# Optimization experiments

Measured on AMD Instinct MI355X. Metric: run time of the kernel, lower is better.

The kernel has to match this reference:

```python
import jax, jax.numpy as jnp
import numpy as np

B, S, D, H = 4, 1024, 512, 8
DH = D // H  # d_head = 64
SQRT_DIM = float(np.sqrt(D))


def _rel_shift(pos_score):
    # pos_score: [B, H, S1, S2] -> Transformer-XL relative shift
    b, h, s1, s2 = pos_score.shape
    padded = jnp.pad(pos_score, ((0, 0), (0, 0), (0, 0), (1, 0)))  # [B,H,S1,S2+1]
    padded = padded.reshape(b, h, s2 + 1, s1)
    return padded[:, :, 1:].reshape(b, h, s1, s2)


def setup_inputs() -> dict:
    key = jax.random.key(0)
    ks = jax.random.split(key, 16)
    p = lambda k, shape: (jax.random.normal(k, shape, dtype=jnp.float32) * 0.02)
    inp = {
        "inputs_1": jax.random.normal(ks[0], (B, S, D), dtype=jnp.float32),
        "inputs_2": jax.random.normal(ks[1], (B, S, D), dtype=jnp.float32),
        "pos_embedding": jax.random.normal(ks[2], (B, S, D), dtype=jnp.float32),
        "mask": jnp.zeros((B, 1, S), dtype=bool),
        "Wq": p(ks[3], (D, H * DH)), "bq": jnp.zeros((H * DH,), jnp.float32),
        "Wk": p(ks[4], (D, H * DH)), "bk": jnp.zeros((H * DH,), jnp.float32),
        "Wv": p(ks[5], (D, H * DH)), "bv": jnp.zeros((H * DH,), jnp.float32),
        "Wp": p(ks[6], (D, D)),  # pos_proj, no bias
        "u_bias": p(ks[7], (H, DH)),
        "v_bias": p(ks[8], (H, DH)),
        "Wo1": p(ks[9], (D, D)), "bo1": jnp.zeros((D,), jnp.float32),
        "Wo2": p(ks[10], (D, D)), "bo2": jnp.zeros((D,), jnp.float32),
    }
    return inp


def _stream(x, pos, mask, Wq, bq, Wk, bk, Wv, bv, u_bias, v_bias, Wo, bo):
    b = x.shape[0]
    q = (x @ Wq + bq).reshape(b, -1, H, DH)          # [B,S,H,dh]
    k = (x @ Wk + bk).reshape(b, -1, H, DH)          # [B,S,H,dh]
    v = (x @ Wv + bv).reshape(b, -1, H, DH)          # [B,S,H,dh]
    content = jnp.einsum("bshd,bthd->bhst", q + u_bias, k)
    pos_score = jnp.einsum("bshd,bthd->bhst", q + v_bias, pos)
    pos_score = _rel_shift(pos_score)
    score = (content + pos_score) / SQRT_DIM          # [B,H,S,S]
    if mask is not None:
        score = jnp.where(mask[:, None], -1e9, score)  # mask: [B,1,S]->[B,1,1,S]
    attn = jax.nn.softmax(score, axis=-1)
    ctx = jnp.einsum("bhst,bthd->bshd", attn, v).reshape(b, -1, D)
    ctx = ctx @ Wo + bo
    return ctx, attn


def reference(inputs_1, inputs_2, pos_embedding, mask, Wq, bq, Wk, bk, Wv, bv,
              Wp, u_bias, v_bias, Wo1, bo1, Wo2, bo2):
    b = inputs_1.shape[0]
    pos = (pos_embedding @ Wp).reshape(b, -1, H, DH)  # [B,S,H,dh]
    # NOTE: original torch code uses value_proj_1 for BOTH streams (value_proj_2 unused)
    ctx1, attn1 = _stream(inputs_1, pos, mask, Wq, bq, Wk, bk, Wv, bv,
                          u_bias, v_bias, Wo1, bo1)
    ctx2, attn2 = _stream(inputs_2, pos, mask, Wq, bq, Wk, bk, Wv, bv,
                          u_bias, v_bias, Wo2, bo2)
    return (ctx1, attn1, ctx2, attn2)
```

## Files before the change

kernel.cpp:

```cpp
#include <hip/hip_runtime.h>
#include <hip/hip_bf16.h>
#include <stdint.h>

typedef __attribute__((ext_vector_type(4))) float f32x4;
typedef __attribute__((ext_vector_type(8))) short bf16x8;

#define OFF_X1B   0UL
#define OFF_X2B   4194304UL
#define OFF_PEB   8388608UL
#define OFF_WQT   12582912UL
#define OFF_WKT   13107200UL
#define OFF_WVT   13631488UL
#define OFF_WPT   14155776UL
#define OFF_WO1T  14680064UL
#define OFF_WO2T  15204352UL
#define OFF_QU1   15728640UL
#define OFF_QV1   19922944UL
#define OFF_K1    24117248UL
#define OFF_V1    28311552UL
#define OFF_QU2   32505856UL
#define OFF_QV2   36700160UL
#define OFF_K2    40894464UL
#define OFF_V2    45088768UL
#define OFF_POSP  49283072UL
#define OFF_VT1   53477376UL
#define OFF_VT2   57671680UL
#define OFF_CP1   61865984UL
#define OFF_CP2   66060288UL

#define CTX1_OFF  0UL
#define ATTN1_OFF 2097152UL
#define CTX2_OFF  35651584UL
#define ATTN2_OFF 37748736UL

struct PP {
  const float* x1; const float* x2; const float* pe; const unsigned char* mask;
  const float* Wq; const float* bq; const float* Wk; const float* bk;
  const float* Wv; const float* bv; const float* Wp;
  const float* ub; const float* vb;
  const float* Wo1; const float* bo1; const float* Wo2; const float* bo2;
  float* out; char* ws;
};

__device__ __forceinline__ short f2bf(float f){
  union { float f; unsigned u; } v; v.f = f;
  unsigned r = v.u + 0x7FFFu + ((v.u >> 16) & 1u);
  return (short)(r >> 16);
}
__device__ __forceinline__ float bf2f(short s){
  union { unsigned u; float f; } v; v.u = ((unsigned)(unsigned short)s) << 16;
  return v.f;
}

__global__ __launch_bounds__(256) void k_cvt(PP p){
  int z = blockIdx.y;
  const float* s = (z==0) ? p.x1 : (z==1) ? p.x2 : p.pe;
  short* d = (short*)(p.ws + (z==0 ? OFF_X1B : z==1 ? OFF_X2B : OFF_PEB));
  size_t i = ((size_t)(blockIdx.x*256 + threadIdx.x))*8;
  float4 a = *(const float4*)(s+i);
  float4 b = *(const float4*)(s+i+4);
  bf16x8 o;
  o[0]=f2bf(a.x); o[1]=f2bf(a.y); o[2]=f2bf(a.z); o[3]=f2bf(a.w);
  o[4]=f2bf(b.x); o[5]=f2bf(b.y); o[6]=f2bf(b.z); o[7]=f2bf(b.w);
  *(bf16x8*)(d+i) = o;
}

__global__ __launch_bounds__(256) void k_cvtw(PP p){
  int z = blockIdx.y;
  const float* src = (z==0)?p.Wq:(z==1)?p.Wk:(z==2)?p.Wv:(z==3)?p.Wp:(z==4)?p.Wo1:p.Wo2;
  short* dst = (short*)(p.ws + ((z==0)?OFF_WQT:(z==1)?OFF_WKT:(z==2)?OFF_WVT:(z==3)?OFF_WPT:(z==4)?OFF_WO1T:OFF_WO2T));
  int tile = blockIdx.x;
  int k0 = (tile & 7)*64, n0 = (tile >> 3)*64;
  __shared__ short tl[64][68];
  int t = threadIdx.x;
  int i = t>>2, jc = (t&3)*16;
  const float* s = src + (size_t)(k0+i)*512 + n0 + jc;
  #pragma unroll
  for (int q=0;q<16;q+=4){
    float4 v = *(const float4*)(s+q);
    tl[i][jc+q+0]=f2bf(v.x); tl[i][jc+q+1]=f2bf(v.y);
    tl[i][jc+q+2]=f2bf(v.z); tl[i][jc+q+3]=f2bf(v.w);
  }
  __syncthreads();
  int n = t>>2, kp2 = (t&3)*16;
  bf16x8 o0, o1;
  #pragma unroll
  for (int q=0;q<8;q++){ o0[q] = tl[kp2+q][n]; o1[q] = tl[kp2+8+q][n]; }
  short* dp = dst + (size_t)(n0+n)*512 + k0 + kp2;
  *(bf16x8*)dp = o0;
  *(bf16x8*)(dp+8) = o1;
}

__global__ __launch_bounds__(256) void k_gemm(PP p, int job_base){
  const int job = job_base + blockIdx.z;
  char* ws = p.ws;
  const short *A, *BT; const float* bias = nullptr;
  short* o0 = nullptr; const float* eb0 = nullptr;
  short* o1 = nullptr; const float* eb1 = nullptr;
  float* of = nullptr;
  switch(job){
    case 0: A=(const short*)(ws+OFF_X1B); BT=(const short*)(ws+OFF_WQT); bias=p.bq;
            o0=(short*)(ws+OFF_QU1); eb0=p.ub; o1=(short*)(ws+OFF_QV1); eb1=p.vb; break;
    case 1: A=(const short*)(ws+OFF_X1B); BT=(const short*)(ws+OFF_WKT); bias=p.bk; o0=(short*)(ws+OFF_K1); break;
    case 2: A=(const short*)(ws+OFF_X1B); BT=(const short*)(ws+OFF_WVT); bias=p.bv; o0=(short*)(ws+OFF_V1); break;
    case 3: A=(const short*)(ws+OFF_X2B); BT=(const short*)(ws+OFF_WQT); bias=p.bq;
            o0=(short*)(ws+OFF_QU2); eb0=p.ub; o1=(short*)(ws+OFF_QV2); eb1=p.vb; break;
    case 4: A=(const short*)(ws+OFF_X2B); BT=(const short*)(ws+OFF_WKT); bias=p.bk; o0=(short*)(ws+OFF_K2); break;
    case 5: A=(const short*)(ws+OFF_X2B); BT=(const short*)(ws+OFF_WVT); bias=p.bv; o0=(short*)(ws+OFF_V2); break;
    case 6: A=(const short*)(ws+OFF_PEB); BT=(const short*)(ws+OFF_WPT); o0=(short*)(ws+OFF_POSP); break;
    case 7: A=(const short*)(ws+OFF_CP1); BT=(const short*)(ws+OFF_WO1T); bias=p.bo1; of=p.out + CTX1_OFF; break;
    default: A=(const short*)(ws+OFF_CP2); BT=(const short*)(ws+OFF_WO2T); bias=p.bo2; of=p.out + CTX2_OFF; break;
  }
  __shared__ short As[128][72];
  __shared__ short Bs[128][72];
  const int t = threadIdx.x, w = t>>6, l = t&63, g = l>>4, r = l&15;
  const int m0 = blockIdx.x*128, n0 = blockIdx.y*128;
  const int wm = (w>>1)*64, wn = (w&1)*64;
  f32x4 acc[4][4];
  #pragma unroll
  for (int i=0;i<4;i++)
    #pragma unroll
    for(int j=0;j<4;j++) acc[i][j] = (f32x4){0.f,0.f,0.f,0.f};

  for (int k0=0; k0<512; k0+=64){
    __syncthreads();
    #pragma unroll
    for (int i=0;i<4;i++){
      int c = t + 256*i;
      int row = c>>3, kc = (c&7)*8;
      *(bf16x8*)&As[row][kc] = *(const bf16x8*)(A + (size_t)(m0+row)*512 + k0 + kc);
      *(bf16x8*)&Bs[row][kc] = *(const bf16x8*)(BT + (size_t)(n0+row)*512 + k0 + kc);
    }
    __syncthreads();
    #pragma unroll
    for (int kk=0; kk<64; kk+=32){
      bf16x8 a[4], bb[4];
      #pragma unroll
      for (int i=0;i<4;i++) a[i] = *(const bf16x8*)&As[wm+16*i+r][kk+8*g];
      #pragma unroll
      for (int j=0;j<4;j++) bb[j] = *(const bf16x8*)&Bs[wn+16*j+r][kk+8*g];
      #pragma unroll
      for (int i=0;i<4;i++)
        #pragma unroll
        for (int j=0;j<4;j++)
          acc[i][j] = __builtin_amdgcn_mfma_f32_16x16x32_bf16(a[i], bb[j], acc[i][j], 0,0,0);
    }
  }
  #pragma unroll
  for (int i=0;i<4;i++){
    #pragma unroll
    for (int j=0;j<4;j++){
      int col = n0 + wn + 16*j + r;
      float bv = bias ? bias[col] : 0.f;
      float e0 = eb0 ? eb0[col] : 0.f;
      float e1 = eb1 ? eb1[col] : 0.f;
      #pragma unroll
      for (int rr=0; rr<4; rr++){
        size_t row = (size_t)(m0 + wm + 16*i + 4*g + rr);
        float val = acc[i][j][rr] + bv;
        if (of) of[row*512 + col] = val;
        else {
          o0[row*512 + col] = f2bf(val + e0);
          if (o1) o1[row*512 + col] = f2bf(val + e1);
        }
      }
    }
  }
}

__global__ __launch_bounds__(256) void k_vtrans(PP p){
  int stile = blockIdx.x, bh = blockIdx.y, st = blockIdx.z;
  const short* v = (const short*)(p.ws + (st? OFF_V2:OFF_V1));
  short* vT = (short*)(p.ws + (st? OFF_VT2:OFF_VT1));
  int b = bh>>3, h = bh&7;
  __shared__ short tl[64][68];
  int t = threadIdx.x;
  int i = t>>2, jc = (t&3)*16;
  const short* src = v + ((size_t)(b*1024 + stile*64 + i))*512 + h*64 + jc;
  *(bf16x8*)&tl[i][jc]   = *(const bf16x8*)src;
  *(bf16x8*)&tl[i][jc+8] = *(const bf16x8*)(src+8);
  __syncthreads();
  int d = t>>2, sp = (t&3)*16;
  bf16x8 o0, o1;
  #pragma unroll
  for (int q=0;q<8;q++){ o0[q]=tl[sp+q][d]; o1[q]=tl[sp+8+q][d]; }
  short* dp = vT + ((size_t)(bh*64 + d))*1024 + stile*64 + sp;
  *(bf16x8*)dp = o0;
  *(bf16x8*)(dp+8) = o1;
}

__global__ __launch_bounds__(256) void k_attn(PP p){
  const int t = threadIdx.x, w = t>>6, l = t&63, g = l>>4, r = l&15;
  const int qt = blockIdx.x, bh = blockIdx.y, st = blockIdx.z;
  const int b = bh>>3, h = bh&7;
  const int r0 = qt*16;
  char* ws = p.ws;
  const short* qu = (const short*)(ws + (st? OFF_QU2:OFF_QU1));
  const short* qv = (const short*)(ws + (st? OFF_QV2:OFF_QV1));
  const short* kp = (const short*)(ws + (st? OFF_K2:OFF_K1));
  const short* vT = (const short*)(ws + (st? OFF_VT2:OFF_VT1));
  short* cp = (short*)(ws + (st? OFF_CP2:OFF_CP1));
  float* attn_out = p.out + (st? ATTN2_OFF : ATTN1_OFF);
  const short* posp = (const short*)(ws + OFF_POSP);

  union ScBuf { short ps[17][1024]; float sc[16][1024]; };
  __shared__ ScBuf u;

  bf16x8 aqu[2], aqv[2], aqv2[2];
  {
    size_t base = ((size_t)(b*1024 + r0 + r))*512 + h*64 + 8*g;
    int row2 = r0 + 16 + r; if (row2 > 1023) row2 = 1023;
    size_t base2 = ((size_t)(b*1024 + row2))*512 + h*64 + 8*g;
    #pragma unroll
    for (int ks=0; ks<2; ks++){
      aqu[ks]  = *(const bf16x8*)(qu + base  + ks*32);
      aqv[ks]  = *(const bf16x8*)(qv + base  + ks*32);
      aqv2[ks] = *(const bf16x8*)(qv + base2 + ks*32);
    }
  }

  {
    size_t pbase = ((size_t)(b*1024))*512 + h*64 + 8*g;
    #pragma unroll 4
    for (int tt=0; tt<16; tt++){
      int n = 256*w + 16*tt;
      f32x4 a0 = {0.f,0.f,0.f,0.f}, a1 = {0.f,0.f,0.f,0.f};
      #pragma unroll
      for (int ks=0; ks<2; ks++){
        bf16x8 bf = *(const bf16x8*)(posp + pbase + (size_t)(n + r)*512 + ks*32);
        a0 = __builtin_amdgcn_mfma_f32_16x16x32_bf16(aqv[ks],  bf, a0, 0,0,0);
        a1 = __builtin_amdgcn_mfma_f32_16x16x32_bf16(aqv2[ks], bf, a1, 0,0,0);
      }
      #pragma unroll
      for (int rr=0; rr<4; rr++) u.ps[4*g+rr][n+r] = f2bf(a0[rr]);
      if (g==0) u.ps[16][n+r] = f2bf(a1[0]);
    }
  }
  __syncthreads();

  f32x4 sca[16];
  {
    size_t kbase = ((size_t)(b*1024))*512 + h*64 + 8*g;
    const unsigned char* mk = p.mask + b*1024;
    #pragma unroll 4
    for (int tt=0; tt<16; tt++){
      int n = 256*w + 16*tt;
      f32x4 a0 = {0.f,0.f,0.f,0.f};
      #pragma unroll
      for (int ks=0; ks<2; ks++){
        bf16x8 bf = *(const bf16x8*)(kp + kbase + (size_t)(n + r)*512 + ks*32);
        a0 = __builtin_amdgcn_mfma_f32_16x16x32_bf16(aqu[ks], bf, a0, 0,0,0);
      }
      int s2 = n + r;
      bool msk = (mk[s2] != 0);
      #pragma unroll
      for (int rr=0; rr<4; rr++){
        int lr = 4*g + rr;
        int s1 = r0 + lr;
        float pv;
        if (s2 <= s1)        pv = bf2f(u.ps[lr][s2 + 1023 - s1]);
        else if (s2 == s1+1) pv = 0.f;
        else                 pv = bf2f(u.ps[lr+1][s2 - s1 - 2]);
        float sv = (a0[rr] + pv) * 0.04419417382415922f;
        if (msk) sv = -1e9f;
        sca[tt][rr] = sv;
      }
    }
  }
  __syncthreads();

  #pragma unroll
  for (int tt=0; tt<16; tt++){
    int s2 = 256*w + 16*tt + r;
    #pragma unroll
    for (int rr=0; rr<4; rr++){
      int row = 4*g + rr;
      u.sc[row][s2 ^ ((row&7)<<3)] = sca[tt][rr];
    }
  }
  __syncthreads();

  #pragma unroll
  for (int rr=0; rr<4; rr++){
    int row = 4*w + rr;
    int sw = (row&7)<<3;
    float vals[16];
    float mx = -1e30f;
    #pragma unroll
    for (int j=0;j<16;j++){
      vals[j] = u.sc[row][(l + 64*j) ^ sw];
      mx = fmaxf(mx, vals[j]);
    }
    #pragma unroll
    for (int off=32; off>0; off>>=1) mx = fmaxf(mx, __shfl_xor(mx, off));
    float s = 0.f;
    #pragma unroll
    for (int j=0;j<16;j++){ vals[j] = __expf(vals[j]-mx); s += vals[j]; }
    #pragma unroll
    for (int off=32; off>0; off>>=1) s += __shfl_xor(s, off);
    float inv = 1.f / s;
    size_t gb = (((size_t)(b*8 + h))*1024 + (size_t)(r0 + row))*1024;
    #pragma unroll
    for (int j=0;j<16;j++){
      float a = vals[j]*inv;
      u.sc[row][(l + 64*j) ^ sw] = a;
      attn_out[gb + l + 64*j] = a;
    }
  }
  __syncthreads();

  {
    f32x4 acc = {0.f,0.f,0.f,0.f};
    const short* vrow = vT + ((size_t)(bh*64 + 16*w + r))*1024;
    int sw = (r&7)<<3;
    for (int k0=0; k0<1024; k0+=32){
      int kb = (k0 + 8*g) ^ sw;
      const float* ap = &u.sc[r][kb];
      f32x4 f0 = *(const f32x4*)ap;
      f32x4 f1 = *(const f32x4*)(ap+4);
      bf16x8 af;
      af[0]=f2bf(f0[0]); af[1]=f2bf(f0[1]); af[2]=f2bf(f0[2]); af[3]=f2bf(f0[3]);
      af[4]=f2bf(f1[0]); af[5]=f2bf(f1[1]); af[6]=f2bf(f1[2]); af[7]=f2bf(f1[3]);
      bf16x8 bf = *(const bf16x8*)(vrow + k0 + 8*g);
      acc = __builtin_amdgcn_mfma_f32_16x16x32_bf16(af, bf, acc, 0,0,0);
    }
    size_t obase = ((size_t)(b*1024 + r0))*512 + (size_t)(h*64 + 16*w + r);
    #pragma unroll
    for (int rr=0; rr<4; rr++)
      cp[obase + (size_t)(4*g+rr)*512] = f2bf(acc[rr]);
  }
}

extern "C" void kernel_launch(void* const* d_in, const int* in_sizes, int n_in,
                              void* d_out, int out_size, void* d_ws, size_t ws_size,
                              hipStream_t stream){
  PP p;
  p.x1  = (const float*)d_in[0];
  p.x2  = (const float*)d_in[1];
  p.pe  = (const float*)d_in[2];
  p.mask= (const unsigned char*)d_in[3];
  p.Wq  = (const float*)d_in[4];  p.bq = (const float*)d_in[5];
  p.Wk  = (const float*)d_in[6];  p.bk = (const float*)d_in[7];
  p.Wv  = (const float*)d_in[8];  p.bv = (const float*)d_in[9];
  p.Wp  = (const float*)d_in[10];
  p.ub  = (const float*)d_in[11]; p.vb = (const float*)d_in[12];
  p.Wo1 = (const float*)d_in[13]; p.bo1= (const float*)d_in[14];
  p.Wo2 = (const float*)d_in[15]; p.bo2= (const float*)d_in[16];
  p.out = (float*)d_out;
  p.ws  = (char*)d_ws;

  hipLaunchKernelGGL(k_cvt,    dim3(1024,3), dim3(256), 0, stream, p);
  hipLaunchKernelGGL(k_cvtw,   dim3(64,6),   dim3(256), 0, stream, p);
  hipLaunchKernelGGL(k_gemm,   dim3(32,4,7), dim3(256), 0, stream, p, 0);
  hipLaunchKernelGGL(k_vtrans, dim3(16,32,2),dim3(256), 0, stream, p);
  hipLaunchKernelGGL(k_attn,   dim3(64,32,2),dim3(256), 0, stream, p);
  hipLaunchKernelGGL(k_gemm,   dim3(32,4,2), dim3(256), 0, stream, p, 7);
}
```

Before: 657.2 us.

## Fuse content and position MFMAs, keep softmax in registers, store probabilities as bf16 in LDS

Computes the content score (q+u)·k in the same loop as the positional score, so k and pos tiles are loaded together. Softmax now runs directly on the MFMA accumulator registers, using shuffle plus a small LDS cross-wave reduction instead of staging a 64KB float score buffer through shared memory. The normalized probabilities are written to global with nontemporal stores and stored as bf16 into the reused swizzled pos buffer, so the PV MFMA loads bf16 operands directly. This shrinks LDS from 64KB to about 34KB, which should allow more resident blocks, and removes one barrier-and-copy stage. The cost is higher register pressure from full unrolling.

```diff
diff --git a/kernel.cpp b/kernel.cpp
--- a/kernel.cpp
+++ b/kernel.cpp
@@ -203,8 +203,10 @@
   float* attn_out = p.out + (st? ATTN2_OFF : ATTN1_OFF);
   const short* posp = (const short*)(ws + OFF_POSP);
 
-  union ScBuf { short ps[17][1024]; float sc[16][1024]; };
-  __shared__ ScBuf u;
+  __shared__ short ps[17*1024];
+  __shared__ float red[2][4][16];
+
+  #define PSI(row,col) ((row)*1024 + ((col) ^ (((row)&7)<<3)))
 
   bf16x8 aqu[2], aqv[2], aqv2[2];
   {
@@ -219,92 +221,114 @@
     }
   }
 
+  f32x4 sca[16];
   {
     size_t pbase = ((size_t)(b*1024))*512 + h*64 + 8*g;
-    #pragma unroll 4
+    #pragma unroll
     for (int tt=0; tt<16; tt++){
       int n = 256*w + 16*tt;
-      f32x4 a0 = {0.f,0.f,0.f,0.f}, a1 = {0.f,0.f,0.f,0.f};
+      f32x4 c0 = {0.f,0.f,0.f,0.f}, p0 = {0.f,0.f,0.f,0.f}, p1 = {0.f,0.f,0.f,0.f};
       #pragma unroll
       for (int ks=0; ks<2; ks++){
-        bf16x8 bf = *(const bf16x8*)(posp + pbase + (size_t)(n + r)*512 + ks*32);
-        a0 = __builtin_amdgcn_mfma_f32_16x16x32_bf16(aqv[ks],  bf, a0, 0,0,0);
-        a1 = __builtin_amdgcn_mfma_f32_16x16x32_bf16(aqv2[ks], bf, a1, 0,0,0);
+        size_t off = pbase + (size_t)(n + r)*512 + ks*32;
+        bf16x8 pf = *(const bf16x8*)(posp + off);
+        bf16x8 kf = *(const bf16x8*)(kp + off);
+        p0 = __builtin_amdgcn_mfma_f32_16x16x32_bf16(aqv[ks],  pf, p0, 0,0,0);
+        p1 = __builtin_amdgcn_mfma_f32_16x16x32_bf16(aqv2[ks], pf, p1, 0,0,0);
+        c0 = __builtin_amdgcn_mfma_f32_16x16x32_bf16(aqu[ks],  kf, c0, 0,0,0);
       }
-      #pragma unroll
-      for (int rr=0; rr<4; rr++) u.ps[4*g+rr][n+r] = f2bf(a0[rr]);
-      if (g==0) u.ps[16][n+r] = f2bf(a1[0]);
-    }
-  }
-  __syncthreads();
-
-  f32x4 sca[16];
-  {
-    size_t kbase = ((size_t)(b*1024))*512 + h*64 + 8*g;
+      sca[tt] = c0;
+      #pragma unroll
+      for (int rr=0; rr<4; rr++) ps[PSI(4*g+rr, n+r)] = f2bf(p0[rr]);
+      if (g==0) ps[PSI(16, n+r)] = f2bf(p1[0]);
+    }
+  }
+  __syncthreads();
+
+  {
     const unsigned char* mk = p.mask + b*1024;
-    #pragma unroll 4
+    #pragma unroll
     for (int tt=0; tt<16; tt++){
       int n = 256*w + 16*tt;
-      f32x4 a0 = {0.f,0.f,0.f,0.f};
-      #pragma unroll
-      for (int ks=0; ks<2; ks++){
-        bf16x8 bf = *(const bf16x8*)(kp + kbase + (size_t)(n + r)*512 + ks*32);
-        a0 = __builtin_amdgcn_mfma_f32_16x16x32_bf16(aqu[ks], bf, a0, 0,0,0);
-      }
       int s2 = n + r;
       bool msk = (mk[s2] != 0);
       #pragma unroll
       for (int rr=0; rr<4; rr++){
-        int lr = 4*g + rr;
-        int s1 = r0 + lr;
+        int lr = 4*g + rr, s1 = r0 + lr;
         float pv;
-        if (s2 <= s1)        pv = bf2f(u.ps[lr][s2 + 1023 - s1]);
+        if (s2 <= s1)        pv = bf2f(ps[PSI(lr, s2 + 1023 - s1)]);
         else if (s2 == s1+1) pv = 0.f;
-        else                 pv = bf2f(u.ps[lr+1][s2 - s1 - 2]);
-        float sv = (a0[rr] + pv) * 0.04419417382415922f;
+        else                 pv = bf2f(ps[PSI(lr+1, s2 - s1 - 2)]);
+        float sv = (sca[tt][rr] + pv) * 0.04419417382415922f;
         if (msk) sv = -1e9f;
         sca[tt][rr] = sv;
       }
     }
   }
-  __syncthreads();
-
+
+  float mx[4];
+  #pragma unroll
+  for (int rr=0; rr<4; rr++){
+    float m_ = -1e30f;
+    #pragma unroll
+    for (int tt=0; tt<16; tt++) m_ = fmaxf(m_, sca[tt][rr]);
+    mx[rr] = m_;
+  }
+  #pragma unroll
+  for (int off=1; off<16; off<<=1){
+    #pragma unroll
+    for (int rr=0; rr<4; rr++) mx[rr] = fmaxf(mx[rr], __shfl_xor(mx[rr], off));
+  }
+  if (r==0){
+    #pragma unroll
+    for (int rr=0; rr<4; rr++) red[0][w][4*g+rr] = mx[rr];
+  }
+  __syncthreads();
+  #pragma unroll
+  for (int rr=0; rr<4; rr++){
+    int lr = 4*g + rr;
+    mx[rr] = fmaxf(fmaxf(red[0][0][lr], red[0][1][lr]),
+                   fmaxf(red[0][2][lr], red[0][3][lr]));
+  }
+  float sm[4] = {0.f,0.f,0.f,0.f};
   #pragma unroll
   for (int tt=0; tt<16; tt++){
-    int s2 = 256*w + 16*tt + r;
     #pragma unroll
     for (int rr=0; rr<4; rr++){
-      int row = 4*g + rr;
-      u.sc[row][s2 ^ ((row&7)<<3)] = sca[tt][rr];
-    }
-  }
-  __syncthreads();
-
+      float e = __expf(sca[tt][rr] - mx[rr]);
+      sca[tt][rr] = e;
+      sm[rr] += e;
+    }
+  }
+  #pragma unroll
+  for (int off=1; off<16; off<<=1){
+    #pragma unroll
+    for (int rr=0; rr<4; rr++) sm[rr] += __shfl_xor(sm[rr], off);
+  }
+  if (r==0){
+    #pragma unroll
+    for (int rr=0; rr<4; rr++) red[1][w][4*g+rr] = sm[rr];
+  }
+  __syncthreads();
+  float inv[4];
   #pragma unroll
   for (int rr=0; rr<4; rr++){
-    int row = 4*w + rr;
-    int sw = (row&7)<<3;
-    float vals[16];
-    float mx = -1e30f;
-    #pragma unroll
-    for (int j=0;j<16;j++){
-      vals[j] = u.sc[row][(l + 64*j) ^ sw];
-      mx = fmaxf(mx, vals[j]);
-    }
-    #pragma unroll
-    for (int off=32; off>0; off>>=1) mx = fmaxf(mx, __shfl_xor(mx, off));
-    float s = 0.f;
-    #pragma unroll
-    for (int j=0;j<16;j++){ vals[j] = __expf(vals[j]-mx); s += vals[j]; }
-    #pragma unroll
-    for (int off=32; off>0; off>>=1) s += __shfl_xor(s, off);
-    float inv = 1.f / s;
-    size_t gb = (((size_t)(b*8 + h))*1024 + (size_t)(r0 + row))*1024;
-    #pragma unroll
-    for (int j=0;j<16;j++){
-      float a = vals[j]*inv;
-      u.sc[row][(l + 64*j) ^ sw] = a;
-      attn_out[gb + l + 64*j] = a;
+    int lr = 4*g + rr;
+    inv[rr] = 1.f / (red[1][0][lr] + red[1][1][lr] + red[1][2][lr] + red[1][3][lr]);
+  }
+
+  {
+    size_t gbase = ((size_t)(b*8 + h))*1048576 + (size_t)r0*1024;
+    #pragma unroll
+    for (int tt=0; tt<16; tt++){
+      int n = 256*w + 16*tt;
+      #pragma unroll
+      for (int rr=0; rr<4; rr++){
+        int lr = 4*g + rr;
+        float a = sca[tt][rr] * inv[rr];
+        __builtin_nontemporal_store(a, &attn_out[gbase + (size_t)lr*1024 + n + r]);
+        ps[PSI(lr, n + r)] = f2bf(a);
+      }
     }
   }
   __syncthreads();
@@ -312,15 +336,9 @@
   {
     f32x4 acc = {0.f,0.f,0.f,0.f};
     const short* vrow = vT + ((size_t)(bh*64 + 16*w + r))*1024;
-    int sw = (r&7)<<3;
+    #pragma unroll 8
     for (int k0=0; k0<1024; k0+=32){
-      int kb = (k0 + 8*g) ^ sw;
-      const float* ap = &u.sc[r][kb];
-      f32x4 f0 = *(const f32x4*)ap;
-      f32x4 f1 = *(const f32x4*)(ap+4);
-      bf16x8 af;
-      af[0]=f2bf(f0[0]); af[1]=f2bf(f0[1]); af[2]=f2bf(f0[2]); af[3]=f2bf(f0[3]);
-      af[4]=f2bf(f1[0]); af[5]=f2bf(f1[1]); af[6]=f2bf(f1[2]); af[7]=f2bf(f1[3]);
+      bf16x8 af = *(const bf16x8*)&ps[PSI(r, k0 + 8*g)];
       bf16x8 bf = *(const bf16x8*)(vrow + k0 + 8*g);
       acc = __builtin_amdgcn_mfma_f32_16x16x32_bf16(af, bf, acc, 0,0,0);
     }
@@ -329,6 +347,7 @@
     for (int rr=0; rr<4; rr++)
       cp[obase + (size_t)(4*g+rr)*512] = f2bf(acc[rr]);
   }
+  #undef PSI
 }
 
 extern "C" void kernel_launch(void* const* d_in, const int* in_sizes, int n_in,
```

New measurement: 720.1 us. 9.6% more time.
